# Kernel tuning notes

Measured on AMD Instinct MI355X. Metric: run time of the kernel, lower is better.

Reference implementation:

```python
import jax, jax.numpy as jnp
import numpy as np

N, E, H, C = 100000, 800000, 128, 128


def setup_inputs() -> dict:
    key = jax.random.key(0)
    ks = jax.random.split(key, 8)
    x = jax.random.normal(ks[0], (N, H), dtype=jnp.float32)
    edge_index = jax.random.randint(ks[1], (2, E), 0, N, dtype=jnp.int32)
    s = 0.02
    w_lead = jax.random.normal(ks[2], (H,), dtype=jnp.float32) * s
    b_lead = jnp.zeros((), dtype=jnp.float32)
    w1 = jax.random.normal(ks[3], (H, H), dtype=jnp.float32) * s
    b1 = jnp.zeros((H,), dtype=jnp.float32)
    w2 = jax.random.normal(ks[4], (H, C), dtype=jnp.float32) * s
    b2 = jnp.zeros((C,), dtype=jnp.float32)
    return {"x": x, "edge_index": edge_index, "w_lead": w_lead, "b_lead": b_lead,
            "w1": w1, "b1": b1, "w2": w2, "b2": b2}


def reference(x, edge_index, w_lead, b_lead, w1, b1, w2, b2):
    num_nodes = x.shape[0]
    row, col = edge_index[0], edge_index[1]
    ar = jnp.arange(num_nodes, dtype=row.dtype)

    # leader election logits per node
    logits = x @ w_lead + b_lead  # [N]

    # extended edge list with self loops (guarantees every squad non-empty)
    src_ext = jnp.concatenate([row, ar])
    dst_ext = jnp.concatenate([col, ar])

    # scatter_max over incoming edges: per-dst max logit, argmax = winning src node
    e_logit = logits[src_ext]
    seg_max = jax.ops.segment_max(e_logit, dst_ext, num_segments=num_nodes)
    cand = jnp.where(e_logit == seg_max[dst_ext], src_ext, -1)
    leader_idx = jax.ops.segment_max(cand, dst_ext, num_segments=num_nodes)
    leader_idx = jnp.where(leader_idx < 0, ar, leader_idx)  # empty-squad fallback: self

    # scatter_mean neighbor aggregation (original edges only)
    sums = jax.ops.segment_sum(x[row], col, num_segments=num_nodes)  # [N,H]
    cnt = jax.ops.segment_sum(jnp.ones_like(col, dtype=x.dtype), col, num_segments=num_nodes)
    neigh_mean = sums / jnp.maximum(cnt, 1.0)[:, None]

    # squad report MLP (computed densely; only leader rows are ever gathered,
    # identical math to the masked-subset version in the original)
    h = jax.nn.gelu(neigh_mean @ w1 + b1, approximate=False)
    reports = h @ w2 + b2  # [N,C]

    # each agent reads its squad leader's report
    return reports[leader_idx]
```

## Files before the change

kernel.cpp:

```cpp
#include <hip/hip_runtime.h>
#include <math.h>

#define H128 128
#define NBLK 64
#define BKT 256
#define MAXNB 512

typedef short bf16x8 __attribute__((ext_vector_type(8)));
typedef unsigned short u16x8 __attribute__((ext_vector_type(8)));
typedef float f32x4 __attribute__((ext_vector_type(4)));

__device__ __forceinline__ unsigned long long enc64(double d) {
    unsigned long long b = (unsigned long long)__double_as_longlong(d);
    return (b & 0x8000000000000000ULL) ? ~b : (b | 0x8000000000000000ULL);
}

__device__ __forceinline__ unsigned short f2bf(float f) {
    unsigned u = __float_as_uint(f);
    return (unsigned short)((u + 0x7FFFu + ((u >> 16) & 1u)) >> 16);
}

__device__ __forceinline__ float bf2f(unsigned short b) {
    return __uint_as_float((unsigned)b << 16);
}

__global__ void k_prep(const float* __restrict__ x, const float* __restrict__ wl,
                       const float* __restrict__ bl, unsigned short* __restrict__ xb,
                       double* __restrict__ logits, int N) {
    int wave = (int)((blockIdx.x * (unsigned)blockDim.x + threadIdx.x) >> 6);
    int lane = threadIdx.x & 63;
    if (wave >= N) return;
    const float2 v = *reinterpret_cast<const float2*>(x + (size_t)wave * H128 + lane * 2);
    const float2 w = *reinterpret_cast<const float2*>(wl + lane * 2);
    unsigned p = (unsigned)f2bf(v.x) | ((unsigned)f2bf(v.y) << 16);
    *reinterpret_cast<unsigned*>(xb + (size_t)wave * H128 + lane * 2) = p;
    double s = (double)v.x * (double)w.x + (double)v.y * (double)w.y;
#pragma unroll
    for (int off = 32; off > 0; off >>= 1) s += __shfl_down(s, off);
    if (lane == 0) logits[wave] = s + (double)bl[0];
}

__global__ __launch_bounds__(256) void k_bhist(const int* __restrict__ dsts,
        int* __restrict__ histg, int E, int NB) {
    __shared__ int h[MAXNB];
    for (int i = threadIdx.x; i < NB; i += 256) h[i] = 0;
    __syncthreads();
    int per = (E + NBLK - 1) / NBLK;
    int s = blockIdx.x * per;
    int e = min(E, s + per);
    for (int j = s + threadIdx.x; j < e; j += 256)
        atomicAdd(&h[dsts[j] >> 8], 1);
    __syncthreads();
    for (int i = threadIdx.x; i < NB; i += 256)
        histg[i * NBLK + blockIdx.x] = h[i];
}

__global__ __launch_bounds__(MAXNB) void k_bscan(const int* __restrict__ histg,
        int* __restrict__ bstart, int NB) {
    __shared__ int sm[MAXNB];
    int t = threadIdx.x;
    int s = 0;
    if (t < NB) {
        const int4* p = reinterpret_cast<const int4*>(histg + t * NBLK);
#pragma unroll
        for (int i = 0; i < NBLK / 4; ++i) { int4 v = p[i]; s += v.x + v.y + v.z + v.w; }
    }
    sm[t] = s;
    __syncthreads();
    for (int o = 1; o < MAXNB; o <<= 1) {
        int add = (t >= o) ? sm[t - o] : 0;
        __syncthreads();
        sm[t] += add;
        __syncthreads();
    }
    if (t == 0) bstart[0] = 0;
    if (t < NB) bstart[t + 1] = sm[t];
}

__global__ void k_base(const int* __restrict__ histg, const int* __restrict__ bstart,
                       int* __restrict__ base, int NB) {
    int b = blockIdx.x * blockDim.x + threadIdx.x;
    if (b >= NB) return;
    const int4* hp = reinterpret_cast<const int4*>(histg + b * NBLK);
    int acc = bstart[b];
    int4* bp = reinterpret_cast<int4*>(base + b * NBLK);
#pragma unroll
    for (int i = 0; i < NBLK / 4; ++i) {
        int4 h = hp[i];
        int4 o;
        o.x = acc; acc += h.x;
        o.y = acc; acc += h.y;
        o.z = acc; acc += h.z;
        o.w = acc; acc += h.w;
        bp[i] = o;
    }
}

__global__ __launch_bounds__(256) void k_binscatter(const int* __restrict__ srcs,
        const int* __restrict__ dsts, const int* __restrict__ base,
        int2* __restrict__ binned, int E, int NB) {
    __shared__ int cur[MAXNB];
    for (int i = threadIdx.x; i < NB; i += 256)
        cur[i] = base[i * NBLK + blockIdx.x];
    __syncthreads();
    int per = (E + NBLK - 1) / NBLK;
    int s = blockIdx.x * per;
    int e = min(E, s + per);
    for (int j = s + threadIdx.x; j < e; j += 256) {
        int d = dsts[j], r = srcs[j];
        int pos = atomicAdd(&cur[d >> 8], 1);
        binned[pos] = make_int2(d, r);
    }
}

__global__ __launch_bounds__(BKT) void k_localize(const int2* __restrict__ binned,
        const int* __restrict__ bstart, int* __restrict__ starts,
        int* __restrict__ csr, int N, int E, int NB) {
    __shared__ int deg[BKT];
    __shared__ int sm[BKT];
    __shared__ int cur[BKT];
    int b = blockIdx.x, t = threadIdx.x;
    int s0 = bstart[b], s1 = bstart[b + 1];
    deg[t] = 0;
    __syncthreads();
    for (int j = s0 + t; j < s1; j += BKT)
        atomicAdd(&deg[binned[j].x & (BKT - 1)], 1);
    __syncthreads();
    int v = deg[t];
    sm[t] = v;
    __syncthreads();
    for (int o = 1; o < BKT; o <<= 1) {
        int add = (t >= o) ? sm[t - o] : 0;
        __syncthreads();
        sm[t] += add;
        __syncthreads();
    }
    int excl = sm[t] - v;
    cur[t] = excl;
    int d = b * BKT + t;
    if (d < N) starts[d] = s0 + excl;
    if (b == NB - 1 && t == 0) starts[N] = E;
    __syncthreads();
    for (int j = s0 + t; j < s1; j += BKT) {
        int2 p = binned[j];
        int pos = atomicAdd(&cur[p.x & (BKT - 1)], 1);
        csr[s0 + pos] = p.y;
    }
}

__global__ __launch_bounds__(256) void k_aggregate(const int* __restrict__ starts,
        const int* __restrict__ csr, const unsigned short* __restrict__ xb,
        const double* __restrict__ logits, unsigned short* __restrict__ meanb,
        int* __restrict__ leader, int N) {
    int d = blockIdx.x * 16 + (threadIdx.x >> 4);
    int lane = threadIdx.x & 15;
    if (d >= N) return;
    int s = starts[d], e = starts[d + 1];
    const unsigned short* xp = xb + lane * 8;
    float a[8];
#pragma unroll
    for (int i = 0; i < 8; ++i) a[i] = 0.f;
    int j = s;
    for (; j + 4 <= e; j += 4) {
        int r0 = csr[j], r1 = csr[j + 1], r2 = csr[j + 2], r3 = csr[j + 3];
        u16x8 v0 = *reinterpret_cast<const u16x8*>(xp + (size_t)r0 * H128);
        u16x8 v1 = *reinterpret_cast<const u16x8*>(xp + (size_t)r1 * H128);
        u16x8 v2 = *reinterpret_cast<const u16x8*>(xp + (size_t)r2 * H128);
        u16x8 v3 = *reinterpret_cast<const u16x8*>(xp + (size_t)r3 * H128);
#pragma unroll
        for (int i = 0; i < 8; ++i)
            a[i] += (bf2f(v0[i]) + bf2f(v1[i])) + (bf2f(v2[i]) + bf2f(v3[i]));
    }
    for (; j < e; ++j) {
        int r0 = csr[j];
        u16x8 v0 = *reinterpret_cast<const u16x8*>(xp + (size_t)r0 * H128);
#pragma unroll
        for (int i = 0; i < 8; ++i) a[i] += bf2f(v0[i]);
    }
    unsigned long long best; int bsrc;
    if (lane == 0) { best = enc64(logits[d]); bsrc = d; }
    else { best = 0ULL; bsrc = -1; }
    for (int k2 = s + lane; k2 < e; k2 += 16) {
        int r = csr[k2];
        unsigned long long lg = enc64(logits[r]);
        if (lg > best || (lg == best && r > bsrc)) { best = lg; bsrc = r; }
    }
#pragma unroll
    for (int o = 8; o > 0; o >>= 1) {
        unsigned long long ob = __shfl_xor(best, o);
        int os = __shfl_xor(bsrc, o);
        if (ob > best || (ob == best && os > bsrc)) { best = ob; bsrc = os; }
    }
    if (lane == 0) leader[d] = bsrc;
    float inv = 1.0f / fmaxf((float)(e - s), 1.0f);
    u16x8 mo;
#pragma unroll
    for (int i = 0; i < 8; ++i) mo[i] = f2bf(a[i] * inv);
    *reinterpret_cast<u16x8*>(meanb + (size_t)d * H128 + lane * 8) = mo;
}

__global__ __launch_bounds__(256, 2) void k_gemm_mfma(
        const unsigned short* __restrict__ A, const float* __restrict__ W,
        const float* __restrict__ bias, const int* __restrict__ leader,
        float* __restrict__ outf, unsigned short* __restrict__ outb,
        int N, int dogelu) {
    __shared__ unsigned short wlT[128][136];
    for (int i = threadIdx.x; i < 4096; i += 256) {
        int k = i >> 5;
        int n4 = (i & 31) * 4;
        float4 w = reinterpret_cast<const float4*>(W)[i];
        wlT[n4 + 0][k] = f2bf(w.x);
        wlT[n4 + 1][k] = f2bf(w.y);
        wlT[n4 + 2][k] = f2bf(w.z);
        wlT[n4 + 3][k] = f2bf(w.w);
    }
    __syncthreads();

    const int wid = threadIdx.x >> 6;
    const int lane = threadIdx.x & 63;
    const int row0 = blockIdx.x * 128 + wid * 32;
    const int kblk = (lane >> 4) * 8;

    int rows[2];
#pragma unroll
    for (int t = 0; t < 2; ++t) {
        int node = row0 + t * 16 + (lane & 15);
        int r = (node < N) ? node : (N - 1);
        if (leader) r = leader[r];
        rows[t] = r;
    }

    bf16x8 xf[2][4];
#pragma unroll
    for (int t = 0; t < 2; ++t)
#pragma unroll
        for (int s = 0; s < 4; ++s)
            xf[t][s] = *reinterpret_cast<const bf16x8*>(A + (size_t)rows[t] * H128 + s * 32 + kblk);

    f32x4 acc[2][8];
#pragma unroll
    for (int t = 0; t < 2; ++t)
#pragma unroll
        for (int cb = 0; cb < 8; ++cb)
#pragma unroll
            for (int j = 0; j < 4; ++j) acc[t][cb][j] = 0.0f;

#pragma unroll
    for (int cb = 0; cb < 8; ++cb) {
        const int ch = cb * 16 + (lane & 15);
#pragma unroll
        for (int s = 0; s < 4; ++s) {
            bf16x8 wf = *reinterpret_cast<bf16x8*>(&wlT[ch][s * 32 + kblk]);
            acc[0][cb] = __builtin_amdgcn_mfma_f32_16x16x32_bf16(wf, xf[0][s], acc[0][cb], 0, 0, 0);
            acc[1][cb] = __builtin_amdgcn_mfma_f32_16x16x32_bf16(wf, xf[1][s], acc[1][cb], 0, 0, 0);
        }
    }

    const int chq = (lane >> 4) * 4;
#pragma unroll
    for (int cb = 0; cb < 8; ++cb) {
        const float4 bv = *reinterpret_cast<const float4*>(&bias[cb * 16 + chq]);
#pragma unroll
        for (int t = 0; t < 2; ++t) {
            int node = row0 + t * 16 + (lane & 15);
            if (node >= N) continue;
            float o[4];
            o[0] = acc[t][cb][0] + bv.x;
            o[1] = acc[t][cb][1] + bv.y;
            o[2] = acc[t][cb][2] + bv.z;
            o[3] = acc[t][cb][3] + bv.w;
            if (dogelu) {
#pragma unroll
                for (int j = 0; j < 4; ++j)
                    o[j] = 0.5f * o[j] * (1.0f + erff(o[j] * 0.70710678118654752440f));
            }
            if (outb) {
                ushort4 ov;
                ov.x = f2bf(o[0]); ov.y = f2bf(o[1]); ov.z = f2bf(o[2]); ov.w = f2bf(o[3]);
                *reinterpret_cast<ushort4*>(outb + (size_t)node * H128 + cb * 16 + chq) = ov;
            } else {
                *reinterpret_cast<float4*>(outf + (size_t)node * H128 + cb * 16 + chq) =
                    make_float4(o[0], o[1], o[2], o[3]);
            }
        }
    }
}

extern "C" void kernel_launch(void* const* d_in, const int* in_sizes, int n_in,
                              void* d_out, int out_size, void* d_ws, size_t ws_size,
                              hipStream_t stream) {
    const float* x     = (const float*)d_in[0];
    const int*   ei    = (const int*)d_in[1];
    const float* wlead = (const float*)d_in[2];
    const float* blead = (const float*)d_in[3];
    const float* w1    = (const float*)d_in[4];
    const float* b1    = (const float*)d_in[5];
    const float* w2    = (const float*)d_in[6];
    const float* b2    = (const float*)d_in[7];
    float* out = (float*)d_out;

    const int N = in_sizes[0] / H128;
    const int E = in_sizes[1] / 2;
    const int NB = (N + BKT - 1) / BKT;
    const int* srcs = ei;
    const int* dsts = ei + E;

    char* ws = (char*)d_ws;
    size_t off = 0;
    auto alloc = [&](size_t bytes) {
        void* p = ws + off;
        off = (off + bytes + 255) & ~(size_t)255;
        return p;
    };
    unsigned short* xb    = (unsigned short*)alloc((size_t)N * H128 * 2);
    unsigned short* meanb = (unsigned short*)alloc((size_t)N * H128 * 2);
    unsigned short* hbuf  = (unsigned short*)alloc((size_t)N * H128 * 2);
    double* logits = (double*)alloc((size_t)N * 8);
    int* leader = (int*)alloc((size_t)N * 4);
    int* starts = (int*)alloc((size_t)(N + 1) * 4);
    int* csr    = (int*)alloc((size_t)E * 4);
    int2* binned = (int2*)alloc((size_t)E * 8);
    int* histg  = (int*)alloc((size_t)NB * NBLK * 4);
    int* bstart = (int*)alloc((size_t)(NB + 1) * 4);
    int* base   = (int*)alloc((size_t)NB * NBLK * 4);

    k_prep<<<(N + 3) / 4, 256, 0, stream>>>(x, wlead, blead, xb, logits, N);

    k_bhist<<<NBLK, 256, 0, stream>>>(dsts, histg, E, NB);
    k_bscan<<<1, MAXNB, 0, stream>>>(histg, bstart, NB);
    k_base<<<(NB + 255) / 256, 256, 0, stream>>>(histg, bstart, base, NB);
    k_binscatter<<<NBLK, 256, 0, stream>>>(srcs, dsts, base, binned, E, NB);
    k_localize<<<NB, BKT, 0, stream>>>(binned, bstart, starts, csr, N, E, NB);

    k_aggregate<<<(N + 15) / 16, 256, 0, stream>>>(starts, csr, xb, logits, meanb, leader, N);

    k_gemm_mfma<<<(N + 127) / 128, 256, 0, stream>>>(meanb, w1, b1, nullptr, nullptr, hbuf, N, 1);
    k_gemm_mfma<<<(N + 127) / 128, 256, 0, stream>>>(hbuf, w2, b2, leader, out, nullptr, N, 0);
}
```

Measured before the change: 262.1 us.

## Fuse prep with histogram, merge scan/base, pack binned pairs, widen aggregate unroll

Merges the bf16-conversion/logit kernel and the destination histogram into one launch with block-range dispatch, and folds the base-offset computation into the bucket scan kernel, cutting two launches. Binned edges are packed into a single 32-bit word (local dst in the top 8 bits, src in the low 24), halving that intermediate's traffic. The aggregation loop now gathers 8 neighbors per iteration and computes the leader argmax inside the same loop, so the separate pass over csr is dropped. The 24-bit packing caps node indices at about 16M. The fused leader scan changes which lanes evaluate which edges but keeps the same tie-break rule.

```diff
diff --git a/kernel.cpp b/kernel.cpp
--- a/kernel.cpp
+++ b/kernel.cpp
@@ -24,48 +24,50 @@
     return __uint_as_float((unsigned)b << 16);
 }
 
-__global__ void k_prep(const float* __restrict__ x, const float* __restrict__ wl,
-                       const float* __restrict__ bl, unsigned short* __restrict__ xb,
-                       double* __restrict__ logits, int N) {
-    int wave = (int)((blockIdx.x * (unsigned)blockDim.x + threadIdx.x) >> 6);
-    int lane = threadIdx.x & 63;
-    if (wave >= N) return;
-    const float2 v = *reinterpret_cast<const float2*>(x + (size_t)wave * H128 + lane * 2);
-    const float2 w = *reinterpret_cast<const float2*>(wl + lane * 2);
-    unsigned p = (unsigned)f2bf(v.x) | ((unsigned)f2bf(v.y) << 16);
-    *reinterpret_cast<unsigned*>(xb + (size_t)wave * H128 + lane * 2) = p;
-    double s = (double)v.x * (double)w.x + (double)v.y * (double)w.y;
-#pragma unroll
-    for (int off = 32; off > 0; off >>= 1) s += __shfl_down(s, off);
-    if (lane == 0) logits[wave] = s + (double)bl[0];
-}
-
-__global__ __launch_bounds__(256) void k_bhist(const int* __restrict__ dsts,
-        int* __restrict__ histg, int E, int NB) {
+__global__ __launch_bounds__(256) void k_front(const float* __restrict__ x,
+        const float* __restrict__ wl, const float* __restrict__ bl,
+        unsigned short* __restrict__ xb, double* __restrict__ logits,
+        const int* __restrict__ dsts, int* __restrict__ histg,
+        int N, int E, int NB, int PB) {
     __shared__ int h[MAXNB];
-    for (int i = threadIdx.x; i < NB; i += 256) h[i] = 0;
-    __syncthreads();
-    int per = (E + NBLK - 1) / NBLK;
-    int s = blockIdx.x * per;
-    int e = min(E, s + per);
-    for (int j = s + threadIdx.x; j < e; j += 256)
-        atomicAdd(&h[dsts[j] >> 8], 1);
-    __syncthreads();
-    for (int i = threadIdx.x; i < NB; i += 256)
-        histg[i * NBLK + blockIdx.x] = h[i];
-}
-
-__global__ __launch_bounds__(MAXNB) void k_bscan(const int* __restrict__ histg,
-        int* __restrict__ bstart, int NB) {
+    if ((int)blockIdx.x < PB) {
+        int wave = (int)(blockIdx.x * 4 + (threadIdx.x >> 6));
+        int lane = threadIdx.x & 63;
+        if (wave >= N) return;
+        const float2 v = *reinterpret_cast<const float2*>(x + (size_t)wave * H128 + lane * 2);
+        const float2 w = *reinterpret_cast<const float2*>(wl + lane * 2);
+        unsigned p = (unsigned)f2bf(v.x) | ((unsigned)f2bf(v.y) << 16);
+        *reinterpret_cast<unsigned*>(xb + (size_t)wave * H128 + lane * 2) = p;
+        double s = (double)v.x * (double)w.x + (double)v.y * (double)w.y;
+#pragma unroll
+        for (int off = 32; off > 0; off >>= 1) s += __shfl_down(s, off);
+        if (lane == 0) logits[wave] = s + (double)bl[0];
+    } else {
+        int bid = blockIdx.x - PB;
+        for (int i = threadIdx.x; i < NB; i += 256) h[i] = 0;
+        __syncthreads();
+        int per = (E + NBLK - 1) / NBLK;
+        int s = bid * per;
+        int e = min(E, s + per);
+        for (int j = s + threadIdx.x; j < e; j += 256)
+            atomicAdd(&h[dsts[j] >> 8], 1);
+        __syncthreads();
+        for (int i = threadIdx.x; i < NB; i += 256)
+            histg[i * NBLK + bid] = h[i];
+    }
+}
+
+__global__ __launch_bounds__(MAXNB) void k_offsets(const int* __restrict__ histg,
+        int* __restrict__ bstart, int* __restrict__ base, int NB) {
     __shared__ int sm[MAXNB];
     int t = threadIdx.x;
-    int s = 0;
+    int tot = 0;
     if (t < NB) {
         const int4* p = reinterpret_cast<const int4*>(histg + t * NBLK);
 #pragma unroll
-        for (int i = 0; i < NBLK / 4; ++i) { int4 v = p[i]; s += v.x + v.y + v.z + v.w; }
-    }
-    sm[t] = s;
+        for (int i = 0; i < NBLK / 4; ++i) { int4 v = p[i]; tot += v.x + v.y + v.z + v.w; }
+    }
+    sm[t] = tot;
     __syncthreads();
     for (int o = 1; o < MAXNB; o <<= 1) {
         int add = (t >= o) ? sm[t - o] : 0;
@@ -74,31 +76,27 @@
         __syncthreads();
     }
     if (t == 0) bstart[0] = 0;
-    if (t < NB) bstart[t + 1] = sm[t];
-}
-
-__global__ void k_base(const int* __restrict__ histg, const int* __restrict__ bstart,
-                       int* __restrict__ base, int NB) {
-    int b = blockIdx.x * blockDim.x + threadIdx.x;
-    if (b >= NB) return;
-    const int4* hp = reinterpret_cast<const int4*>(histg + b * NBLK);
-    int acc = bstart[b];
-    int4* bp = reinterpret_cast<int4*>(base + b * NBLK);
-#pragma unroll
-    for (int i = 0; i < NBLK / 4; ++i) {
-        int4 h = hp[i];
-        int4 o;
-        o.x = acc; acc += h.x;
-        o.y = acc; acc += h.y;
-        o.z = acc; acc += h.z;
-        o.w = acc; acc += h.w;
-        bp[i] = o;
+    if (t < NB) {
+        bstart[t + 1] = sm[t];
+        int acc = sm[t] - tot;
+        const int4* hp = reinterpret_cast<const int4*>(histg + t * NBLK);
+        int4* bp = reinterpret_cast<int4*>(base + t * NBLK);
+#pragma unroll
+        for (int i = 0; i < NBLK / 4; ++i) {
+            int4 hv = hp[i];
+            int4 o;
+            o.x = acc; acc += hv.x;
+            o.y = acc; acc += hv.y;
+            o.z = acc; acc += hv.z;
+            o.w = acc; acc += hv.w;
+            bp[i] = o;
+        }
     }
 }
 
 __global__ __launch_bounds__(256) void k_binscatter(const int* __restrict__ srcs,
         const int* __restrict__ dsts, const int* __restrict__ base,
-        int2* __restrict__ binned, int E, int NB) {
+        unsigned* __restrict__ binned, int E, int NB) {
     __shared__ int cur[MAXNB];
     for (int i = threadIdx.x; i < NB; i += 256)
         cur[i] = base[i * NBLK + blockIdx.x];
@@ -109,11 +107,11 @@
     for (int j = s + threadIdx.x; j < e; j += 256) {
         int d = dsts[j], r = srcs[j];
         int pos = atomicAdd(&cur[d >> 8], 1);
-        binned[pos] = make_int2(d, r);
-    }
-}
-
-__global__ __launch_bounds__(BKT) void k_localize(const int2* __restrict__ binned,
+        binned[pos] = ((unsigned)(d & (BKT - 1)) << 24) | (unsigned)r;
+    }
+}
+
+__global__ __launch_bounds__(BKT) void k_localize(const unsigned* __restrict__ binned,
         const int* __restrict__ bstart, int* __restrict__ starts,
         int* __restrict__ csr, int N, int E, int NB) {
     __shared__ int deg[BKT];
@@ -124,7 +122,7 @@
     deg[t] = 0;
     __syncthreads();
     for (int j = s0 + t; j < s1; j += BKT)
-        atomicAdd(&deg[binned[j].x & (BKT - 1)], 1);
+        atomicAdd(&deg[binned[j] >> 24], 1);
     __syncthreads();
     int v = deg[t];
     sm[t] = v;
@@ -142,9 +140,9 @@
     if (b == NB - 1 && t == 0) starts[N] = E;
     __syncthreads();
     for (int j = s0 + t; j < s1; j += BKT) {
-        int2 p = binned[j];
-        int pos = atomicAdd(&cur[p.x & (BKT - 1)], 1);
-        csr[s0 + pos] = p.y;
+        unsigned p = binned[j];
+        int pos = atomicAdd(&cur[p >> 24], 1);
+        csr[s0 + pos] = (int)(p & 0xFFFFFFu);
     }
 }
 
@@ -160,30 +158,53 @@
     float a[8];
 #pragma unroll
     for (int i = 0; i < 8; ++i) a[i] = 0.f;
-    int j = s;
-    for (; j + 4 <= e; j += 4) {
-        int r0 = csr[j], r1 = csr[j + 1], r2 = csr[j + 2], r3 = csr[j + 3];
-        u16x8 v0 = *reinterpret_cast<const u16x8*>(xp + (size_t)r0 * H128);
-        u16x8 v1 = *reinterpret_cast<const u16x8*>(xp + (size_t)r1 * H128);
-        u16x8 v2 = *reinterpret_cast<const u16x8*>(xp + (size_t)r2 * H128);
-        u16x8 v3 = *reinterpret_cast<const u16x8*>(xp + (size_t)r3 * H128);
-#pragma unroll
-        for (int i = 0; i < 8; ++i)
-            a[i] += (bf2f(v0[i]) + bf2f(v1[i])) + (bf2f(v2[i]) + bf2f(v3[i]));
-    }
-    for (; j < e; ++j) {
-        int r0 = csr[j];
-        u16x8 v0 = *reinterpret_cast<const u16x8*>(xp + (size_t)r0 * H128);
-#pragma unroll
-        for (int i = 0; i < 8; ++i) a[i] += bf2f(v0[i]);
-    }
+
     unsigned long long best; int bsrc;
     if (lane == 0) { best = enc64(logits[d]); bsrc = d; }
     else { best = 0ULL; bsrc = -1; }
-    for (int k2 = s + lane; k2 < e; k2 += 16) {
-        int r = csr[k2];
-        unsigned long long lg = enc64(logits[r]);
-        if (lg > best || (lg == best && r > bsrc)) { best = lg; bsrc = r; }
+
+    int j = s;
+    for (; j + 8 <= e; j += 8) {
+        int r[8];
+#pragma unroll
+        for (int q = 0; q < 8; ++q) r[q] = csr[j + q];
+        u16x8 v[8];
+#pragma unroll
+        for (int q = 0; q < 8; ++q)
+            v[q] = *reinterpret_cast<const u16x8*>(xp + (size_t)r[q] * H128);
+#pragma unroll
+        for (int i = 0; i < 8; ++i)
+            a[i] += ((bf2f(v[0][i]) + bf2f(v[1][i])) + (bf2f(v[2][i]) + bf2f(v[3][i])))
+                  + ((bf2f(v[4][i]) + bf2f(v[5][i])) + (bf2f(v[6][i]) + bf2f(v[7][i])));
+        if (lane < 8) {
+            int rr = r[lane];
+            unsigned long long lg = enc64(logits[rr]);
+            if (lg > best || (lg == best && rr > bsrc)) { best = lg; bsrc = rr; }
+        }
+    }
+    for (; j + 2 <= e; j += 2) {
+        int r0 = csr[j], r1 = csr[j + 1];
+        u16x8 v0 = *reinterpret_cast<const u16x8*>(xp + (size_t)r0 * H128);
+        u16x8 v1 = *reinterpret_cast<const u16x8*>(xp + (size_t)r1 * H128);
+#pragma unroll
+        for (int i = 0; i < 8; ++i) a[i] += bf2f(v0[i]) + bf2f(v1[i]);
+        if (lane == 0) {
+            unsigned long long lg = enc64(logits[r0]);
+            if (lg > best || (lg == best && r0 > bsrc)) { best = lg; bsrc = r0; }
+        } else if (lane == 1) {
+            unsigned long long lg = enc64(logits[r1]);
+            if (lg > best || (lg == best && r1 > bsrc)) { best = lg; bsrc = r1; }
+        }
+    }
+    if (j < e) {
+        int r0 = csr[j];
+        u16x8 v0 = *reinterpret_cast<const u16x8*>(xp + (size_t)r0 * H128);
+#pragma unroll
+        for (int i = 0; i < 8; ++i) a[i] += bf2f(v0[i]);
+        if (lane == 0) {
+            unsigned long long lg = enc64(logits[r0]);
+            if (lg > best || (lg == best && r0 > bsrc)) { best = lg; bsrc = r0; }
+        }
     }
 #pragma unroll
     for (int o = 8; o > 0; o >>= 1) {
@@ -302,6 +323,7 @@
     const int N = in_sizes[0] / H128;
     const int E = in_sizes[1] / 2;
     const int NB = (N + BKT - 1) / BKT;
+    const int PB = (N + 3) / 4;
     const int* srcs = ei;
     const int* dsts = ei + E;
 
@@ -319,16 +341,15 @@
     int* leader = (int*)alloc((size_t)N * 4);
     int* starts = (int*)alloc((size_t)(N + 1) * 4);
     int* csr    = (int*)alloc((size_t)E * 4);
-    int2* binned = (int2*)alloc((size_t)E * 8);
+    unsigned* binned = (unsigned*)alloc((size_t)E * 4);
     int* histg  = (int*)alloc((size_t)NB * NBLK * 4);
     int* bstart = (int*)alloc((size_t)(NB + 1) * 4);
     int* base   = (int*)alloc((size_t)NB * NBLK * 4);
 
-    k_prep<<<(N + 3) / 4, 256, 0, stream>>>(x, wlead, blead, xb, logits, N);
-
-    k_bhist<<<NBLK, 256, 0, stream>>>(dsts, histg, E, NB);
-    k_bscan<<<1, MAXNB, 0, stream>>>(histg, bstart, NB);
-    k_base<<<(NB + 255) / 256, 256, 0, stream>>>(histg, bstart, base, NB);
+    k_front<<<PB + NBLK, 256, 0, stream>>>(x, wlead, blead, xb, logits,
+                                           dsts, histg, N, E, NB, PB);
+
+    k_offsets<<<1, MAXNB, 0, stream>>>(histg, bstart, base, NB);
     k_binscatter<<<NBLK, 256, 0, stream>>>(srcs, dsts, base, binned, E, NB);
     k_localize<<<NB, BKT, 0, stream>>>(binned, bstart, starts, csr, N, E, NB);
 
```

Result: slower. 284.7 us (+8.6%).
